# Kernel tuning notes

Hardware: AMD Instinct MI355X
Metric: run time of the kernel (lower is better)

The kernel has to match this reference:

```python
import jax, jax.numpy as jnp
import numpy as np

EPS_BN = 1e-3   # keras BatchNormalization default epsilon
NUM_HEADS = 8

def _bn(x, g, b, m, v):
    # inference-mode BN over channel axis 1 (channels_first); works for 2D (B,C) too
    shp = (1, -1) + (1,) * (x.ndim - 2)
    return (x - m.reshape(shp)) * jax.lax.rsqrt(v.reshape(shp) + EPS_BN) * g.reshape(shp) + b.reshape(shp)

def _l2n(x):
    # tf.nn.l2_normalize along last axis, epsilon 1e-12
    return x * jax.lax.rsqrt(jnp.maximum(jnp.sum(x * x, axis=-1, keepdims=True), 1e-12))

def _gelu(x):
    return jax.nn.gelu(x, approximate=False)  # keras 'gelu' is exact

def _forward(x, w_qkv, w_proj, b_proj, dw_k, dw_b, dw_gamma, dw_beta, dw_mean, dw_var,
             ci_w1, ci_b1, ci_gamma, ci_beta, ci_mean, ci_var, ci_w2, ci_b2,
             si_w1, si_b1, si_gamma, si_beta, si_mean, si_var, si_w2, si_b2, temperature):
    B, C, H, W = x.shape
    N = H * W
    h = NUM_HEADS
    hd = C // h
    xt = x.reshape(B, C, N).transpose(0, 2, 1)                      # (B,N,C)
    qkv = (xt @ w_qkv).reshape(B, N, 3, h, hd).transpose(2, 0, 3, 1, 4)  # (3,B,h,N,hd)
    q = qkv[0].transpose(0, 1, 3, 2)                                # (B,h,hd,N)
    k = qkv[1].transpose(0, 1, 3, 2)
    v = qkv[2].transpose(0, 1, 3, 2)
    v_img = v.reshape(B, C, H, W)
    # channel-wise (XCA-style) attention: (hd x hd) per head
    attn = jnp.einsum('bhcn,bhdn->bhcd', _l2n(q), _l2n(k)) * temperature  # temperature (h,1,1)
    attn = jax.nn.softmax(attn, axis=-1)
    att = jnp.einsum('bhcd,bhdn->bhcn', attn, v)                    # (B,h,hd,N)
    attened = att.transpose(0, 3, 1, 2).reshape(B, N, C)            # (B,N,C)
    # depthwise conv 3x3 + BN + GELU branch on v
    conv = jax.lax.conv_general_dilated(v_img, dw_k, (1, 1), 'SAME',
                                        feature_group_count=C,
                                        dimension_numbers=('NCHW', 'OIHW', 'NCHW'))
    conv = _gelu(_bn(conv + dw_b[None, :, None, None], dw_gamma, dw_beta, dw_mean, dw_var))
    # channel interaction: GAP(attention map) -> 1x1 convs (as dense)
    gap = attened.mean(axis=1)                                      # (B,C)
    cm = _gelu(_bn(gap @ ci_w1 + ci_b1, ci_gamma, ci_beta, ci_mean, ci_var))
    cm = cm @ ci_w2 + ci_b2                                         # (B,C)
    # spatial interaction on conv branch: 1x1 convs
    sm = jnp.einsum('bchw,co->bohw', conv, si_w1) + si_b1[None, :, None, None]
    sm = _gelu(_bn(sm, si_gamma, si_beta, si_mean, si_var))
    sm = jnp.einsum('bchw,co->bohw', sm, si_w2) + si_b2[None, :, None, None]  # (B,1,H,W)
    sm = sm.reshape(B, N, 1)
    attened = attened * jax.nn.sigmoid(sm)
    conv = conv * jax.nn.sigmoid(cm)[:, :, None, None]
    conv_flat = conv.transpose(0, 2, 3, 1).reshape(B, N, C)
    out = (attened + conv_flat) @ w_proj + b_proj                   # (B,N,C)
    return out.transpose(0, 2, 1).reshape(B, C, H, W)

def setup_inputs() -> dict:
    key = jax.random.key(0)
    ks = jax.random.split(key, 8)
    B, C, H, W = 8, 256, 64, 64
    d = {}
    d['x'] = jax.random.normal(ks[0], (B, C, H, W), jnp.float32)
    d['w_qkv'] = jax.random.normal(ks[1], (C, 3 * C), jnp.float32) * 0.02
    d['w_proj'] = jax.random.normal(ks[2], (C, C), jnp.float32) * 0.02
    d['b_proj'] = jnp.zeros((C,), jnp.float32)
    d['dw_k'] = jax.random.normal(ks[3], (C, 1, 3, 3), jnp.float32) * 0.1
    d['dw_b'] = jnp.zeros((C,), jnp.float32)
    for pre, ch in (('dw', C), ('ci', C // 8), ('si', C // 16)):
        d[pre + '_gamma'] = jnp.ones((ch,), jnp.float32)
        d[pre + '_beta'] = jnp.zeros((ch,), jnp.float32)
        d[pre + '_mean'] = jnp.zeros((ch,), jnp.float32)
        d[pre + '_var'] = jnp.ones((ch,), jnp.float32)
    d['ci_w1'] = jax.random.normal(ks[4], (C, C // 8), jnp.float32) * 0.05
    d['ci_b1'] = jnp.zeros((C // 8,), jnp.float32)
    d['ci_w2'] = jax.random.normal(ks[5], (C // 8, C), jnp.float32) * 0.05
    d['ci_b2'] = jnp.zeros((C,), jnp.float32)
    d['si_w1'] = jax.random.normal(ks[6], (C, C // 16), jnp.float32) * 0.05
    d['si_b1'] = jnp.zeros((C // 16,), jnp.float32)
    d['si_w2'] = jax.random.normal(ks[7], (C // 16, 1), jnp.float32) * 0.05
    d['si_b2'] = jnp.zeros((1,), jnp.float32)
    d['temperature'] = jnp.ones((NUM_HEADS, 1, 1), jnp.float32)
    return d

def reference(x, w_qkv, w_proj, b_proj, dw_k, dw_b, dw_gamma, dw_beta, dw_mean, dw_var,
              ci_w1, ci_b1, ci_gamma, ci_beta, ci_mean, ci_var, ci_w2, ci_b2,
              si_w1, si_b1, si_gamma, si_beta, si_mean, si_var, si_w2, si_b2, temperature):
    return _forward(x, w_qkv, w_proj, b_proj, dw_k, dw_b, dw_gamma, dw_beta, dw_mean, dw_var,
                    ci_w1, ci_b1, ci_gamma, ci_beta, ci_mean, ci_var, ci_w2, ci_b2,
                    si_w1, si_b1, si_gamma, si_beta, si_mean, si_var, si_w2, si_b2, temperature)
```

## Files before the change

### kernel.cpp

```cpp
#include <hip/hip_runtime.h>
#include <hip/hip_bf16.h>
#include <math.h>

typedef __hip_bfloat16 bf16;
typedef __attribute__((ext_vector_type(8))) short short8;
typedef __attribute__((ext_vector_type(4))) short short4v;
typedef __attribute__((ext_vector_type(4))) float floatx4;

__device__ __forceinline__ bf16 f2b(float v) { return __float2bfloat16(v); }
__device__ __forceinline__ short f2s(float v) {
    bf16 h = __float2bfloat16(v);
    return *reinterpret_cast<short*>(&h);
}
__device__ __forceinline__ float s2f(short s) {
    union { unsigned u; float f; } t;
    t.u = ((unsigned)(unsigned short)s) << 16;
    return t.f;
}
__device__ __forceinline__ float gelu_exact(float x) {
    return 0.5f * x * (1.0f + erff(x * 0.70710678118654752440f));
}
__device__ __forceinline__ float sigmoidf_(float x) {
    return 1.0f / (1.0f + __expf(-x));
}
__device__ __forceinline__ float ldin(const void* p, int i, bool isbf) {
    return isbf ? s2f(((const short*)p)[i]) : ((const float*)p)[i];
}
#define MFMA16(a, b, c) __builtin_amdgcn_mfma_f32_16x16x32_bf16(a, b, c, 0, 0, 0)

#define P_DWK    0
#define P_DWB    2304
#define P_DWG    2560
#define P_DWBT   2816
#define P_DWM    3072
#define P_DWV    3328
#define P_CIW1   3584
#define P_CIB1   11776
#define P_CIG    11808
#define P_CIBT   11840
#define P_CIM    11872
#define P_CIV    11904
#define P_CIW2   11936
#define P_CIB2   20128
#define P_SIW1   20384
#define P_SIB1   24480
#define P_SIG    24496
#define P_SIBT   24512
#define P_SIM    24528
#define P_SIV    24544
#define P_SIW2   24560
#define P_SIB2   24576
#define P_TEMP   24577
#define P_BPROJ  24585

__device__ __forceinline__ bool block_sniff(const unsigned* __restrict__ x) {
    int cnt = 0;
    for (int i = threadIdx.x; i < 4096; i += 256) {
        unsigned lo = x[i] & 0xFFFFu;
        unsigned e = (lo >> 7) & 0xFFu;
        cnt += (e >= 0x66u && e <= 0x8Au) ? 1 : 0;
    }
    __shared__ int red[256];
    red[threadIdx.x] = cnt;
    __syncthreads();
    for (int o = 128; o > 0; o >>= 1) {
        if (threadIdx.x < o) red[threadIdx.x] += red[threadIdx.x + o];
        __syncthreads();
    }
    return red[0] > 2048;
}

struct CvtArgs { const void* src[24]; int dst[24]; int cnt[24]; };

__global__ __launch_bounds__(256) void k_prept(CvtArgs a,
                                               const void* __restrict__ x,
                                               const void* __restrict__ wqkv,
                                               const void* __restrict__ wproj,
                                               bf16* __restrict__ xT,
                                               bf16* __restrict__ wqkvT,
                                               bf16* __restrict__ wprojT,
                                               float* __restrict__ prm,
                                               unsigned* __restrict__ flag,
                                               float* __restrict__ accbuf) {
    __shared__ short T[64][72];
    const bool isbf = block_sniff((const unsigned*)x);
    const int id = blockIdx.x;
    const int tid = threadIdx.x;

    if (id >= 2112) {
        int e = id - 2112;
        if (e < 24) {
            const void* s = a.src[e];
            float* d = prm + a.dst[e];
            const int n = a.cnt[e];
            for (int i = tid; i < n; i += 256) d[i] = ldin(s, i, isbf);
        } else {
            for (int i = tid; i < 6144; i += 256) accbuf[i] = 0.f;
            if (tid == 0) *flag = isbf ? 1u : 0u;
        }
        return;
    }

    const int cc = tid >> 3, oct = tid & 7;
    const void* src;
    bf16* dst;
    long row_stride, src_off;
    int c0;
    long out_row_off;
    if (id < 2048) {
        int nx = id & 63, cy = (id >> 6) & 3, b = id >> 8;
        c0 = cy * 64;
        int n0 = nx * 64;
        src = x;
        dst = xT;
        row_stride = 4096;
        src_off = ((long)(b * 256 + c0) << 12) + n0;
        out_row_off = ((long)(b << 12) + n0) << 8;
    } else if (id < 2096) {
        int id2 = id - 2048;
        int jx = id2 % 12, cy = id2 / 12;
        c0 = cy * 64;
        int j0 = jx * 64;
        src = wqkv;
        dst = wqkvT;
        row_stride = 768;
        src_off = (long)c0 * 768 + j0;
        out_row_off = (long)j0 << 8;
    } else {
        int id3 = id - 2096;
        int jx = id3 & 3, cy = id3 >> 2;
        c0 = cy * 64;
        int j0 = jx * 64;
        src = wproj;
        dst = wprojT;
        row_stride = 256;
        src_off = (long)c0 * 256 + j0;
        out_row_off = (long)j0 << 8;
    }

#pragma unroll
    for (int i = 0; i < 2; ++i) {
        int col = cc + i * 32;
        long gbase = src_off + (long)col * row_stride + oct * 8;
        short v[8];
        if (isbf) {
            short8 p = *(const short8*)((const short*)src + gbase);
#pragma unroll
            for (int u = 0; u < 8; ++u) v[u] = p[u];
        } else {
            floatx4 q0 = *(const floatx4*)((const float*)src + gbase);
            floatx4 q1 = *(const floatx4*)((const float*)src + gbase + 4);
#pragma unroll
            for (int u = 0; u < 4; ++u) { v[u] = f2s(q0[u]); v[4 + u] = f2s(q1[u]); }
        }
        int row0 = oct * 8;
#pragma unroll
        for (int u = 0; u < 8; ++u) {
            int row = row0 + u;
            T[row][(((col >> 3) ^ (row & 7)) << 3) + (col & 7)] = v[u];
        }
    }
    __syncthreads();
    const int rr = tid >> 3;
#pragma unroll
    for (int i = 0; i < 2; ++i) {
        int row = rr + i * 32;
        short8 p = *(const short8*)&T[row][((oct ^ (row & 7)) << 3)];
        *(short8*)&dst[out_row_off + ((long)row << 8) + c0 + oct * 8] = p;
    }
}

__global__ __launch_bounds__(256) void k_qkv_m3(const bf16* __restrict__ xT,
                                                const bf16* __restrict__ wT,
                                                bf16* __restrict__ qb,
                                                bf16* __restrict__ kb,
                                                bf16* __restrict__ vbb,
                                                float* __restrict__ qss,
                                                float* __restrict__ kss) {
    __shared__ short As[128][72];
    __shared__ short Bs[128][72];
    const int id = blockIdx.x;
    const int swz = (id & 7) * 192 + (id >> 3);
    const int y = swz % 6;
    const int rest = swz / 6;
    const int n0 = (rest & 31) * 128;
    const int b = rest >> 5;
    const int j0 = y * 128;
    const int tid = threadIdx.x;
    const int wid = tid >> 6, l = tid & 63;
    const int wr = wid >> 1, wc = wid & 1;
    const int lm = l & 15, lk = (l >> 4) * 8;
    const int srow = tid >> 3, soct = tid & 7;
    floatx4 acc[4][4];
#pragma unroll
    for (int i = 0; i < 4; ++i)
#pragma unroll
        for (int j = 0; j < 4; ++j) acc[i][j] = (floatx4){0.f, 0.f, 0.f, 0.f};

    for (int k0 = 0; k0 < 256; k0 += 64) {
        __syncthreads();
#pragma unroll
        for (int i = 0; i < 4; ++i) {
            int row = srow + i * 32;
            *(short8*)&As[row][soct * 8] =
                *(const short8*)&wT[((j0 + row) << 8) + k0 + soct * 8];
            *(short8*)&Bs[row][soct * 8] =
                *(const short8*)&xT[(((b << 12) + n0 + row) << 8) + k0 + soct * 8];
        }
        __syncthreads();
#pragma unroll
        for (int h = 0; h < 2; ++h) {
            short8 af[4], bfv[4];
#pragma unroll
            for (int mt = 0; mt < 4; ++mt)
                af[mt] = *(const short8*)&As[wr * 64 + mt * 16 + lm][h * 32 + lk];
#pragma unroll
            for (int nt = 0; nt < 4; ++nt)
                bfv[nt] = *(const short8*)&Bs[wc * 64 + nt * 16 + lm][h * 32 + lk];
#pragma unroll
            for (int mt = 0; mt < 4; ++mt)
#pragma unroll
                for (int nt = 0; nt < 4; ++nt)
                    acc[mt][nt] = MFMA16(af[mt], bfv[nt], acc[mt][nt]);
        }
    }
    const int jbase = wr * 64 + (l >> 4) * 4;
    const int jq = (y & 1) * 128;
    if (y < 4) {
        bf16* dst = (y < 2) ? qb : kb;
#pragma unroll
        for (int mt = 0; mt < 4; ++mt)
#pragma unroll
            for (int nt = 0; nt < 4; ++nt) {
                int n = n0 + wc * 64 + nt * 16 + lm;
#pragma unroll
                for (int r = 0; r < 4; ++r)
                    dst[(((b << 8) + jq + jbase + mt * 16 + r) << 12) + n] =
                        f2b(acc[mt][nt][r]);
            }
        __syncthreads();
        float* red = (float*)&As[0][0];
#pragma unroll
        for (int mt = 0; mt < 4; ++mt)
#pragma unroll
            for (int r = 0; r < 4; ++r) {
                float s = 0.f;
#pragma unroll
                for (int nt = 0; nt < 4; ++nt) {
                    float v = acc[mt][nt][r];
                    s = fmaf(v, v, s);
                }
                red[(jbase + mt * 16 + r) * 32 + wc * 16 + lm] = s;
            }
        __syncthreads();
        if (tid < 128) {
            float s = 0.f;
#pragma unroll
            for (int i = 0; i < 32; ++i)
                s += red[tid * 32 + ((i + tid) & 31)];
            float* dsts = (y < 2) ? qss : kss;
            atomicAdd(&dsts[(b << 8) + jq + tid], s);
        }
    } else {
#pragma unroll
        for (int mt = 0; mt < 4; ++mt)
#pragma unroll
            for (int nt = 0; nt < 4; ++nt) {
                int n = n0 + wc * 64 + nt * 16 + lm;
#pragma unroll
                for (int r = 0; r < 4; ++r)
                    vbb[(((b << 8) + jq + jbase + mt * 16 + r) << 12) + n] =
                        f2b(acc[mt][nt][r]);
            }
    }
}

__global__ __launch_bounds__(256) void k_qkdw(const bf16* __restrict__ qb,
                                              const bf16* __restrict__ kb,
                                              const float* __restrict__ qss,
                                              const float* __restrict__ kss,
                                              const bf16* __restrict__ vbb,
                                              const float* __restrict__ prm,
                                              float* __restrict__ attn,
                                              bf16* __restrict__ convT) {
    __shared__ __align__(16) char smem[38368];
    const int id = blockIdx.x;
    const int tid = threadIdx.x;
    if (id < 64) {
        float (*AS)[32] = (float(*)[32])smem;
        const int h = id & 7, b = id >> 3;
        const int wid = tid >> 6, l = tid & 63;
        const int lm = l & 15, lk = (l >> 4) * 8;
        floatx4 acc[2][2];
#pragma unroll
        for (int i = 0; i < 2; ++i)
#pragma unroll
            for (int j = 0; j < 2; ++j) acc[i][j] = (floatx4){0.f, 0.f, 0.f, 0.f};
        const int cbase = (b << 8) + h * 32;
        for (int it = 0; it < 32; ++it) {
            int n = wid * 1024 + it * 32 + lk;
            short8 a0 = *(const short8*)&qb[((cbase + lm) << 12) + n];
            short8 a1 = *(const short8*)&qb[((cbase + 16 + lm) << 12) + n];
            short8 b0 = *(const short8*)&kb[((cbase + lm) << 12) + n];
            short8 b1 = *(const short8*)&kb[((cbase + 16 + lm) << 12) + n];
            acc[0][0] = MFMA16(a0, b0, acc[0][0]);
            acc[0][1] = MFMA16(a0, b1, acc[0][1]);
            acc[1][0] = MFMA16(a1, b0, acc[1][0]);
            acc[1][1] = MFMA16(a1, b1, acc[1][1]);
        }
        for (int i = tid; i < 1024; i += 256) ((float*)AS)[i] = 0.f;
        __syncthreads();
#pragma unroll
        for (int mt = 0; mt < 2; ++mt)
#pragma unroll
            for (int nt = 0; nt < 2; ++nt)
#pragma unroll
                for (int r = 0; r < 4; ++r)
                    atomicAdd(&AS[mt * 16 + (l >> 4) * 4 + r][nt * 16 + lm],
                              acc[mt][nt][r]);
        __syncthreads();
        if (tid < 32) {
            const int c = tid;
            float qsc = rsqrtf(fmaxf(qss[cbase + c], 1e-12f)) * prm[P_TEMP + h];
            float row[32];
            float m = -1e30f;
#pragma unroll
            for (int d = 0; d < 32; ++d) {
                row[d] = AS[c][d] * qsc * rsqrtf(fmaxf(kss[cbase + d], 1e-12f));
                m = fmaxf(m, row[d]);
            }
            float s = 0.f;
#pragma unroll
            for (int d = 0; d < 32; ++d) {
                row[d] = __expf(row[d] - m);
                s += row[d];
            }
            float inv = 1.0f / s;
            float* dst = attn + ((b * 8 + h) << 10) + c * 32;
#pragma unroll
            for (int d = 0; d < 32; ++d) dst[d] = row[d] * inv;
        }
    } else {
        float (*S)[18][66] = (float(*)[18][66])smem;
        float (*Wl)[11] = (float(*)[11])(smem + 38016);
        const int id2 = id - 64;
        const int y0 = (id2 & 3) * 16, c0 = ((id2 >> 2) & 31) * 8, b = id2 >> 7;
        if (tid < 144) {
            int ch = tid / 18, r = tid - ch * 18;
            int gy = y0 + r - 1;
            float* drow = &S[ch][r][0];
            if (gy < 0 || gy > 63) {
                for (int i = 0; i < 66; ++i) drow[i] = 0.f;
            } else {
                const short* src = (const short*)vbb +
                                   ((((b << 8) + c0 + ch) << 12) + gy * 64);
                drow[0] = 0.f;
                drow[65] = 0.f;
#pragma unroll
                for (int g = 0; g < 8; ++g) {
                    short8 p = *(const short8*)(src + g * 8);
#pragma unroll
                    for (int u = 0; u < 8; ++u) drow[1 + g * 8 + u] = s2f(p[u]);
                }
            }
        } else if (tid >= 248) {
            int ch = tid - 248;
            int c = c0 + ch;
            float scale = rsqrtf(prm[P_DWV + c] + 1e-3f) * prm[P_DWG + c];
#pragma unroll
            for (int e = 0; e < 9; ++e) Wl[ch][e] = prm[P_DWK + c * 9 + e] * scale;
            Wl[ch][10] = (prm[P_DWB + c] - prm[P_DWM + c]) * scale + prm[P_DWBT + c];
        }
        __syncthreads();
        const int row = tid >> 4, xl = tid & 15;
#pragma unroll
        for (int u = 0; u < 4; ++u) {
            int x = xl + u * 16;
            short8 o;
#pragma unroll
            for (int ch = 0; ch < 8; ++ch) {
                float acc = Wl[ch][10];
#pragma unroll
                for (int ky = 0; ky < 3; ++ky)
#pragma unroll
                    for (int kx = 0; kx < 3; ++kx)
                        acc = fmaf(S[ch][row + ky][x + kx], Wl[ch][ky * 3 + kx], acc);
                o[ch] = f2s(gelu_exact(acc));
            }
            *(short8*)&((short*)convT)[(((b << 12) + (y0 + row) * 64 + x) << 8) + c0] = o;
        }
    }
}

__global__ __launch_bounds__(256) void k_attv_sm(const float* __restrict__ attn,
                                                 const bf16* __restrict__ vbb,
                                                 const bf16* __restrict__ convT,
                                                 const float* __restrict__ prm,
                                                 bf16* __restrict__ attT,
                                                 float* __restrict__ gap,
                                                 float* __restrict__ sigsm) {
    __shared__ __align__(16) char smem[36864];
    const int id = blockIdx.x;
    const int tid = threadIdx.x;
    if (id < 1024) {
        float (*A)[32] = (float(*)[32])smem;
        float (*G)[32] = (float(*)[32])(smem + 4096);
        const int nx = id & 15, h = (id >> 4) & 7, b = id >> 7;
        const int n = nx * 256 + tid;
        for (int i = tid; i < 1024; i += 256)
            ((float*)A)[i] = attn[((b * 8 + h) << 10) + i];
        __syncthreads();
        const int base = ((b * 256 + h * 32) << 12) + n;
        float vv[32];
#pragma unroll
        for (int d = 0; d < 32; ++d) vv[d] = s2f(((const short*)vbb)[base + (d << 12)]);
        float av[32];
#pragma unroll
        for (int c = 0; c < 32; ++c) {
            float s = 0.f;
#pragma unroll
            for (int d = 0; d < 32; ++d) s = fmaf(A[c][d], vv[d], s);
            av[c] = s;
            G[tid][(c + tid) & 31] = s;
        }
        const int obase = (((b << 12) + n) << 8) + h * 32;
#pragma unroll
        for (int g = 0; g < 4; ++g) {
            short8 p;
#pragma unroll
            for (int u = 0; u < 8; ++u) p[u] = f2s(av[g * 8 + u]);
            *(short8*)&attT[obase + g * 8] = p;
        }
        __syncthreads();
        {
            const int colc = tid & 31, rg = tid >> 5;
            float s = 0.f;
#pragma unroll
            for (int i = 0; i < 32; ++i) {
                int row = rg * 32 + i;
                s += G[row][(colc + row) & 31];
            }
            A[rg][colc] = s;
        }
        __syncthreads();
        if (tid < 32) {
            float s = 0.f;
#pragma unroll
            for (int g = 0; g < 8; ++g) s += A[g][tid];
            atomicAdd(&gap[(b << 8) + h * 32 + tid], s);
        }
    } else {
        float (*W1)[16] = (float(*)[16])smem;
        const int id2 = id - 1024;
        const int nx = id2 & 15, b = id2 >> 4;
        const int n = nx * 256 + tid;
        for (int i = tid; i < 4096; i += 256) W1[i >> 4][i & 15] = prm[P_SIW1 + i];
        __syncthreads();
        float acc[16];
#pragma unroll
        for (int o = 0; o < 16; ++o) acc[o] = 0.f;
        const bf16* src = convT + (((b << 12) + n) << 8);
#pragma unroll 4
        for (int g = 0; g < 32; ++g) {
            short8 p = *(const short8*)&src[g * 8];
#pragma unroll
            for (int u = 0; u < 8; ++u) {
                float v = s2f(p[u]);
                int c = g * 8 + u;
#pragma unroll
                for (int o = 0; o < 16; ++o) acc[o] = fmaf(v, W1[c][o], acc[o]);
            }
        }
        float sm = prm[P_SIB2];
#pragma unroll
        for (int o = 0; o < 16; ++o) {
            float t = acc[o] + prm[P_SIB1 + o];
            t = (t - prm[P_SIM + o]) * rsqrtf(prm[P_SIV + o] + 1e-3f) * prm[P_SIG + o] +
                prm[P_SIBT + o];
            sm = fmaf(gelu_exact(t), prm[P_SIW2 + o], sm);
        }
        sigsm[(b << 12) + n] = sigmoidf_(sm);
    }
}

__global__ __launch_bounds__(256) void k_proj_m3(const bf16* __restrict__ attT,
                                                 const bf16* __restrict__ convT,
                                                 const float* __restrict__ sigsm,
                                                 const float* __restrict__ gap,
                                                 const bf16* __restrict__ wpT,
                                                 const float* __restrict__ prm,
                                                 const unsigned* __restrict__ flag,
                                                 void* __restrict__ out) {
    __shared__ short As[128][72];
    __shared__ short Bs[128][72];
    __shared__ float scs[256];
    const bool isbf = (*flag != 0u);
    const int id = blockIdx.x;
    const int swz = (id & 7) * 64 + (id >> 3);
    const int j0 = (swz & 1) * 128;
    const int rest = swz >> 1;
    const int n0 = (rest & 31) * 128;
    const int b = rest >> 5;
    const int tid = threadIdx.x;
    const int wid = tid >> 6, l = tid & 63;
    const int wr = wid >> 1, wc = wid & 1;
    const int lm = l & 15, lk = (l >> 4) * 8;
    const int srow = tid >> 3, soct = tid & 7;

    {
        float* gl = (float*)&As[0][0];
        float* rd = gl + 256;
        float* t1 = rd + 256;
        gl[tid] = gap[(b << 8) + tid] * (1.0f / 4096.0f);
        __syncthreads();
        const int o = tid >> 3, g = tid & 7;
        float s1 = 0.f;
#pragma unroll
        for (int i = 0; i < 32; ++i) {
            int c = g * 32 + i;
            s1 = fmaf(gl[c], prm[P_CIW1 + c * 32 + o], s1);
        }
        rd[o * 8 + g] = s1;
        __syncthreads();
        if (tid < 32) {
            float s = prm[P_CIB1 + tid];
#pragma unroll
            for (int g2 = 0; g2 < 8; ++g2) s += rd[tid * 8 + g2];
            s = (s - prm[P_CIM + tid]) * rsqrtf(prm[P_CIV + tid] + 1e-3f) *
                    prm[P_CIG + tid] + prm[P_CIBT + tid];
            t1[tid] = gelu_exact(s);
        }
        __syncthreads();
        float s = prm[P_CIB2 + tid];
#pragma unroll
        for (int o2 = 0; o2 < 32; ++o2)
            s = fmaf(t1[o2], prm[P_CIW2 + o2 * 256 + tid], s);
        scs[tid] = sigmoidf_(s);
    }

    floatx4 acc[4][4];
#pragma unroll
    for (int i = 0; i < 4; ++i)
#pragma unroll
        for (int j = 0; j < 4; ++j) acc[i][j] = (floatx4){0.f, 0.f, 0.f, 0.f};

    for (int k0 = 0; k0 < 256; k0 += 64) {
        __syncthreads();
#pragma unroll
        for (int i = 0; i < 4; ++i) {
            int row = srow + i * 32;
            *(short8*)&As[row][soct * 8] =
                *(const short8*)&wpT[((j0 + row) << 8) + k0 + soct * 8];
            int rbase = (((b << 12) + n0 + row) << 8) + k0 + soct * 8;
            short8 pa = *(const short8*)&attT[rbase];
            short8 pc = *(const short8*)&convT[rbase];
            float sv = sigsm[(b << 12) + n0 + row];
            short8 pz;
#pragma unroll
            for (int u = 0; u < 8; ++u)
                pz[u] = f2s(s2f(pa[u]) * sv + s2f(pc[u]) * scs[k0 + soct * 8 + u]);
            *(short8*)&Bs[row][soct * 8] = pz;
        }
        __syncthreads();
#pragma unroll
        for (int h = 0; h < 2; ++h) {
            short8 af[4], bfv[4];
#pragma unroll
            for (int mt = 0; mt < 4; ++mt)
                af[mt] = *(const short8*)&As[wr * 64 + mt * 16 + lm][h * 32 + lk];
#pragma unroll
            for (int nt = 0; nt < 4; ++nt)
                bfv[nt] = *(const short8*)&Bs[wc * 64 + nt * 16 + lm][h * 32 + lk];
#pragma unroll
            for (int mt = 0; mt < 4; ++mt)
#pragma unroll
                for (int nt = 0; nt < 4; ++nt)
                    acc[mt][nt] = MFMA16(af[mt], bfv[nt], acc[mt][nt]);
        }
    }
    const int jbase = j0 + wr * 64 + (l >> 4) * 4;
#pragma unroll
    for (int mt = 0; mt < 4; ++mt) {
        float bp[4];
#pragma unroll
        for (int r = 0; r < 4; ++r) bp[r] = prm[P_BPROJ + jbase + mt * 16 + r];
#pragma unroll
        for (int nt = 0; nt < 4; ++nt) {
            int n = n0 + wc * 64 + nt * 16 + lm;
#pragma unroll
            for (int r = 0; r < 4; ++r) {
                int idx = (((b << 8) + jbase + mt * 16 + r) << 12) + n;
                float val = acc[mt][nt][r] + bp[r];
                if (isbf) ((bf16*)out)[idx] = f2b(val);
                else ((float*)out)[idx] = val;
            }
        }
    }
}

extern "C" void kernel_launch(void* const* d_in, const int* in_sizes, int n_in,
                              void* d_out, int out_size, void* d_ws, size_t ws_size,
                              hipStream_t stream) {
    char* ws = (char*)d_ws;
    bf16*  vbb    = (bf16*) (ws);
    bf16*  xT     = (bf16*) (ws + 33554432);
    bf16*  attT   = (bf16*) (ws + 33554432);
    bf16*  qb     = (bf16*) (ws + 50331648);
    bf16*  kb     = (bf16*) (ws + 67108864);
    bf16*  wqkvT  = (bf16*) (ws + 83886080);
    bf16*  wprojT = (bf16*) (ws + 84279296);
    float* attn   = (float*)(ws + 84410368);
    float* qss    = (float*)(ws + 85721088);
    float* kss    = (float*)(ws + 85729280);
    float* gap    = (float*)(ws + 85737472);
    float* sigsm  = (float*)(ws + 85753856);
    float* prm    = (float*)(ws + 85884928);
    unsigned* flag = (unsigned*)(ws + 85985280);
    bf16*  convT  = (bf16*) (ws + 100663296);

    CvtArgs a;
    const int map_src[24] = {3, 4, 5, 6, 7, 8, 9, 10, 11, 12, 13, 14, 15, 16, 17,
                             18, 19, 20, 21, 22, 23, 24, 25, 26};
    const int map_dst[24] = {P_BPROJ, P_DWK, P_DWB, P_DWG, P_DWBT, P_DWM, P_DWV,
                             P_CIG, P_CIBT, P_CIM, P_CIV, P_SIG, P_SIBT, P_SIM, P_SIV,
                             P_CIW1, P_CIB1, P_CIW2, P_CIB2, P_SIW1, P_SIB1, P_SIW2,
                             P_SIB2, P_TEMP};
    for (int i = 0; i < 24; ++i) {
        a.src[i] = d_in[map_src[i]];
        a.dst[i] = map_dst[i];
        a.cnt[i] = in_sizes[map_src[i]];
    }

    k_prept<<<2137, 256, 0, stream>>>(a, d_in[0], d_in[1], d_in[2],
                                      xT, wqkvT, wprojT, prm, flag, qss);
    k_qkv_m3<<<1536, 256, 0, stream>>>(xT, wqkvT, qb, kb, vbb, qss, kss);
    k_qkdw<<<1088, 256, 0, stream>>>(qb, kb, qss, kss, vbb, prm, attn, convT);
    k_attv_sm<<<1152, 256, 0, stream>>>(attn, vbb, convT, prm, attT, gap, sigsm);
    k_proj_m3<<<512, 256, 0, stream>>>(attT, convT, sigsm, gap,
                                       wprojT, prm, flag, d_out);
}
```

Baseline: 133.3 us.

## Write transposed V copy in QKV GEMM and use MFMA for attn@V

The QKV GEMM epilogue now also writes V in an (N,C) transposed bf16 layout alongside the existing channel-major copy. The attn@V stage reads this transposed V with vector loads and computes the 32x32 head product with bf16 MFMA instead of scalar FP32 FMAs. It stages the result through shared memory for coalesced stores and reduces GAP sums with shared atomics. The cost is an extra V write of about 16MB, and the attention matrix is now rounded to bf16 before the product.

```diff
diff --git a/kernel.cpp b/kernel.cpp
--- a/kernel.cpp
+++ b/kernel.cpp
@@ -175,6 +175,7 @@
                                                 bf16* __restrict__ qb,
                                                 bf16* __restrict__ kb,
                                                 bf16* __restrict__ vbb,
+                                                bf16* __restrict__ vT,
                                                 float* __restrict__ qss,
                                                 float* __restrict__ kss) {
     __shared__ short As[128][72];
@@ -267,10 +268,15 @@
 #pragma unroll
             for (int nt = 0; nt < 4; ++nt) {
                 int n = n0 + wc * 64 + nt * 16 + lm;
-#pragma unroll
-                for (int r = 0; r < 4; ++r)
-                    vbb[(((b << 8) + jq + jbase + mt * 16 + r) << 12) + n] =
-                        f2b(acc[mt][nt][r]);
+                short4v pv;
+#pragma unroll
+                for (int r = 0; r < 4; ++r) {
+                    float vf = acc[mt][nt][r];
+                    vbb[(((b << 8) + jq + jbase + mt * 16 + r) << 12) + n] = f2b(vf);
+                    pv[r] = f2s(vf);
+                }
+                *(short4v*)&((short*)vT)[(((long)(b << 12) + n) << 8) +
+                                         jq + jbase + mt * 16] = pv;
             }
     }
 }
@@ -393,62 +399,69 @@
 }
 
 __global__ __launch_bounds__(256) void k_attv_sm(const float* __restrict__ attn,
-                                                 const bf16* __restrict__ vbb,
+                                                 const bf16* __restrict__ vT,
                                                  const bf16* __restrict__ convT,
                                                  const float* __restrict__ prm,
                                                  bf16* __restrict__ attT,
                                                  float* __restrict__ gap,
                                                  float* __restrict__ sigsm) {
-    __shared__ __align__(16) char smem[36864];
+    __shared__ __align__(16) char smem[20608];
     const int id = blockIdx.x;
     const int tid = threadIdx.x;
     if (id < 1024) {
-        float (*A)[32] = (float(*)[32])smem;
-        float (*G)[32] = (float(*)[32])(smem + 4096);
-        const int nx = id & 15, h = (id >> 4) & 7, b = id >> 7;
-        const int n = nx * 256 + tid;
+        float (*P)[32] = (float(*)[32])smem;
+        short (*AT)[32] = (short(*)[32])(smem + 4096);
+        float* gacc = (float*)(smem + 4096 + 16384);
+        const int nq = id & 15, h = (id >> 4) & 7, b = id >> 7;
         for (int i = tid; i < 1024; i += 256)
-            ((float*)A)[i] = attn[((b * 8 + h) << 10) + i];
-        __syncthreads();
-        const int base = ((b * 256 + h * 32) << 12) + n;
-        float vv[32];
-#pragma unroll
-        for (int d = 0; d < 32; ++d) vv[d] = s2f(((const short*)vbb)[base + (d << 12)]);
-        float av[32];
-#pragma unroll
-        for (int c = 0; c < 32; ++c) {
-            float s = 0.f;
-#pragma unroll
-            for (int d = 0; d < 32; ++d) s = fmaf(A[c][d], vv[d], s);
-            av[c] = s;
-            G[tid][(c + tid) & 31] = s;
-        }
-        const int obase = (((b << 12) + n) << 8) + h * 32;
-#pragma unroll
-        for (int g = 0; g < 4; ++g) {
-            short8 p;
-#pragma unroll
-            for (int u = 0; u < 8; ++u) p[u] = f2s(av[g * 8 + u]);
-            *(short8*)&attT[obase + g * 8] = p;
-        }
-        __syncthreads();
-        {
-            const int colc = tid & 31, rg = tid >> 5;
-            float s = 0.f;
-#pragma unroll
-            for (int i = 0; i < 32; ++i) {
-                int row = rg * 32 + i;
-                s += G[row][(colc + row) & 31];
-            }
-            A[rg][colc] = s;
-        }
-        __syncthreads();
-        if (tid < 32) {
-            float s = 0.f;
-#pragma unroll
-            for (int g = 0; g < 8; ++g) s += A[g][tid];
-            atomicAdd(&gap[(b << 8) + h * 32 + tid], s);
-        }
+            ((float*)P)[i] = attn[((b * 8 + h) << 10) + i];
+        if (tid < 32) gacc[tid] = 0.f;
+        __syncthreads();
+        const int w = tid >> 6, l = tid & 63;
+        const int lm = l & 15, lk = (l >> 4) * 8;
+        short8 bfr[2];
+#pragma unroll
+        for (int ct = 0; ct < 2; ++ct) {
+            floatx4 p0 = *(const floatx4*)&P[ct * 16 + lm][lk];
+            floatx4 p1 = *(const floatx4*)&P[ct * 16 + lm][lk + 4];
+#pragma unroll
+            for (int u = 0; u < 4; ++u) {
+                bfr[ct][u] = f2s(p0[u]);
+                bfr[ct][4 + u] = f2s(p1[u]);
+            }
+        }
+        const floatx4 zero = {0.f, 0.f, 0.f, 0.f};
+        const short* vTs = (const short*)vT;
+#pragma unroll
+        for (int t = 0; t < 4; ++t) {
+            int nl = w * 64 + t * 16;
+            int n0 = nq * 256 + nl;
+            short8 afr = *(const short8*)&vTs[(((long)(b << 12) + n0 + lm) << 8) +
+                                              h * 32 + lk];
+            floatx4 d0 = MFMA16(afr, bfr[0], zero);
+            floatx4 d1 = MFMA16(afr, bfr[1], zero);
+            int rowb = nl + (l >> 4) * 4;
+            float s0 = 0.f, s1 = 0.f;
+#pragma unroll
+            for (int r = 0; r < 4; ++r) {
+                AT[rowb + r][lm] = f2s(d0[r]);
+                AT[rowb + r][16 + lm] = f2s(d1[r]);
+                s0 += d0[r];
+                s1 += d1[r];
+            }
+            atomicAdd(&gacc[lm], s0);
+            atomicAdd(&gacc[16 + lm], s1);
+        }
+        __syncthreads();
+        const long gb = ((long)(b << 12) + nq * 256) << 8;
+#pragma unroll
+        for (int q = 0; q < 4; ++q) {
+            int s = tid + q * 256;
+            int row = s >> 2, grp = s & 3;
+            *(short8*)&((short*)attT)[gb + ((long)row << 8) + h * 32 + grp * 8] =
+                *(const short8*)&AT[row][grp * 8];
+        }
+        if (tid < 32) atomicAdd(&gap[(b << 8) + h * 32 + tid], gacc[tid]);
     } else {
         float (*W1)[16] = (float(*)[16])smem;
         const int id2 = id - 1024;
@@ -617,6 +630,7 @@
     float* prm    = (float*)(ws + 85884928);
     unsigned* flag = (unsigned*)(ws + 85985280);
     bf16*  convT  = (bf16*) (ws + 100663296);
+    bf16*  vT     = (bf16*) (ws + 117440512);
 
     CvtArgs a;
     const int map_src[24] = {3, 4, 5, 6, 7, 8, 9, 10, 11, 12, 13, 14, 15, 16, 17,
@@ -633,9 +647,9 @@
 
     k_prept<<<2137, 256, 0, stream>>>(a, d_in[0], d_in[1], d_in[2],
                                       xT, wqkvT, wprojT, prm, flag, qss);
-    k_qkv_m3<<<1536, 256, 0, stream>>>(xT, wqkvT, qb, kb, vbb, qss, kss);
+    k_qkv_m3<<<1536, 256, 0, stream>>>(xT, wqkvT, qb, kb, vbb, vT, qss, kss);
     k_qkdw<<<1088, 256, 0, stream>>>(qb, kb, qss, kss, vbb, prm, attn, convT);
-    k_attv_sm<<<1152, 256, 0, stream>>>(attn, vbb, convT, prm, attT, gap, sigsm);
+    k_attv_sm<<<1152, 256, 0, stream>>>(attn, vT, convT, prm, attT, gap, sigsm);
     k_proj_m3<<<512, 256, 0, stream>>>(attT, convT, sigsm, gap,
                                        wprojT, prm, flag, d_out);
 }
```

Result: no change. 134.3 us (+0.7%).
